# Optimization experiments

Measured on AMD Instinct MI355X. Metric: run time of the kernel, lower is better.

The kernel has to match this reference:

```python
import jax, jax.numpy as jnp
import numpy as np

D_MODEL = 768
D_INNER = 1536      # expand=2
D_STATE = 16
DT_RANK = 48        # ceil(768/16)
D_CONV = 4
DEPTH = 24
NUM_CLASSES = 527
GRID = (8, 64)      # (128/16, 1024/16)
SEQ = GRID[0] * GRID[1]
TOKPOS = SEQ // 2   # middle cls token position


def setup_inputs() -> dict:
    key = jax.random.key(0)
    ks = jax.random.split(key, 12)
    rn = lambda k, s, sc=0.02: jax.random.normal(k, s, jnp.float32) * sc
    A_init = jnp.log(jnp.arange(1, D_STATE + 1, dtype=jnp.float32))  # S4D-real init
    return {
        "x": jax.random.normal(ks[0], (1, 1, 128, 1024), jnp.float32),
        "patch_w": rn(ks[1], (D_MODEL, 1, 16, 16)),
        "patch_b": jnp.zeros((D_MODEL,), jnp.float32),
        "cls_token": rn(ks[2], (1, 1, D_MODEL)),
        "pos_embed": rn(ks[3], (1, SEQ + 1, D_MODEL)),
        "in_proj_w": rn(ks[4], (DEPTH, 2 * D_INNER, D_MODEL)),
        "conv_w": rn(ks[5], (DEPTH, 2, D_INNER, D_CONV), 0.1),
        "conv_b": jnp.zeros((DEPTH, 2, D_INNER), jnp.float32),
        "xproj_w": rn(ks[6], (DEPTH, 2, DT_RANK + 2 * D_STATE, D_INNER)),
        "dtproj_w": rn(ks[7], (DEPTH, 2, D_INNER, DT_RANK), 0.1),
        "dtproj_b": jnp.full((DEPTH, 2, D_INNER), float(np.log(np.expm1(0.01))), jnp.float32),
        "A_log": jnp.ones((DEPTH, 2, D_INNER, 1), jnp.float32) * A_init,
        "D_skip": jnp.ones((DEPTH, 2, D_INNER), jnp.float32),
        "out_proj_w": rn(ks[8], (DEPTH, D_MODEL, D_INNER)),
        "norm_w": jnp.ones((DEPTH, D_MODEL), jnp.float32),
        "norm_f_w": jnp.ones((D_MODEL,), jnp.float32),
        "head_w": rn(ks[9], (NUM_CLASSES, D_MODEL)),
        "head_b": jnp.zeros((NUM_CLASSES,), jnp.float32),
    }


def _rmsnorm(x, w, eps=1e-5):
    return x * jax.lax.rsqrt(jnp.mean(x * x, axis=-1, keepdims=True) + eps) * w


def _causal_conv_silu(x, w, b):
    # x [B,d,L], depthwise causal conv, kernel D_CONV, left-pad D_CONV-1
    L = x.shape[-1]
    xp = jnp.pad(x, ((0, 0), (0, 0), (D_CONV - 1, 0)))
    y = sum(w[:, k, None] * xp[:, :, k:k + L] for k in range(D_CONV)) + b[:, None]
    return jax.nn.silu(y)


def _selective_scan(dt, A, Bm, C, u):
    # dt,u: [B,d,L]; Bm,C: [B,N,L]; A: [d,N] (negative)
    def step(h, inp):
        dt_t, B_t, C_t, u_t = inp           # [B,d],[B,N],[B,N],[B,d]
        h = h * jnp.exp(dt_t[..., None] * A) + (dt_t * u_t)[..., None] * B_t[:, None, :]
        return h, jnp.einsum('bdn,bn->bd', h, C_t)
    h0 = jnp.zeros((dt.shape[0], A.shape[0], A.shape[1]), dt.dtype)
    mv = lambda a: jnp.moveaxis(a, -1, 0)
    _, ys = jax.lax.scan(step, h0, (mv(dt), mv(Bm), mv(C), mv(u)))
    return jnp.moveaxis(ys, 0, -1)          # [B,d,L]


def _mamba_dir(x, z, cw, cb, xw, dw, db, A_log, Dsk):
    xc = _causal_conv_silu(x, cw, cb)
    dbl = jnp.einsum('bdl,cd->bcl', xc, xw)                 # [B, R+2N, L]
    dt = jax.nn.softplus(jnp.einsum('brl,dr->bdl', dbl[:, :DT_RANK], dw) + db[:, None])
    Bm = dbl[:, DT_RANK:DT_RANK + D_STATE]
    C = dbl[:, DT_RANK + D_STATE:]
    y = _selective_scan(dt, -jnp.exp(A_log), Bm, C, xc) + Dsk[:, None] * xc
    return y * jax.nn.silu(z)


def _block(carry, p):
    hidden, residual = carry
    ipw, cw, cb, xw, dw, db, A_log, Dsk, opw, nw = p
    residual = residual + hidden                            # add -> norm -> mixer
    h = _rmsnorm(residual, nw)
    xz = jnp.einsum('bld,ed->ble', h, ipw)                  # [B,L,2*d_inner]
    x, z = jnp.split(jnp.moveaxis(xz, -1, 1), 2, axis=1)    # each [B,d_inner,L]
    yf = _mamba_dir(x, z, cw[0], cb[0], xw[0], dw[0], db[0], A_log[0], Dsk[0])
    yb = _mamba_dir(x[:, :, ::-1], z[:, :, ::-1], cw[1], cb[1], xw[1], dw[1],
                    db[1], A_log[1], Dsk[1])[:, :, ::-1]
    out = jnp.einsum('bdl,ed->ble', (yf + yb) * 0.5, opw)   # if_devide_out
    return (out, residual), None


def reference(x, patch_w, patch_b, cls_token, pos_embed, in_proj_w, conv_w, conv_b,
              xproj_w, dtproj_w, dtproj_b, A_log, D_skip, out_proj_w, norm_w,
              norm_f_w, head_w, head_b):
    h = jax.lax.conv_general_dilated(x, patch_w, (16, 16), 'VALID',
                                     dimension_numbers=('NCHW', 'OIHW', 'NCHW'))
    h = h + patch_b[None, :, None, None]
    B = h.shape[0]
    h = h.reshape(B, D_MODEL, SEQ).transpose(0, 2, 1)       # [B,512,768]
    cls = jnp.broadcast_to(cls_token, (B, 1, D_MODEL))
    h = jnp.concatenate([h[:, :TOKPOS], cls, h[:, TOKPOS:]], axis=1)  # [B,513,768]
    h = h + pos_embed
    carry = (h, jnp.zeros_like(h))
    (hidden, residual), _ = jax.lax.scan(
        _block, carry,
        (in_proj_w, conv_w, conv_b, xproj_w, dtproj_w, dtproj_b, A_log, D_skip,
         out_proj_w, norm_w))
    out = _rmsnorm(residual + hidden, norm_f_w)
    feat = out[:, TOKPOS]                                   # middle cls token
    return feat @ head_w.T + head_b
```

## Files before the change

kernel.cpp:

```cpp
#include <hip/hip_runtime.h>

#define L_SEQ 513
#define DM 768
#define DI 1536
#define DSTATE 16
#define DTRANK 48
#define NCLS 527
#define DEPTH 24
#define NC 32
#define CLEN 17
#define SKI 3
#define SKO 8

typedef unsigned short u16;
typedef __bf16 bf16x8 __attribute__((ext_vector_type(8)));
typedef float f32x4 __attribute__((ext_vector_type(4)));

#define MFMA_BF16(A, B, C) __builtin_amdgcn_mfma_f32_16x16x32_bf16(A, B, C, 0, 0, 0)

__device__ inline u16 f2bf(float x) {
  unsigned u = __float_as_uint(x);
  return (u16)((u + 0x7FFFu + ((u >> 16) & 1u)) >> 16);
}
__device__ inline float bf2f(u16 h) { return __uint_as_float((unsigned)h << 16); }
__device__ inline void split2(float v, u16& h, u16& l) {
  h = f2bf(v);
  l = f2bf(v - bf2f(h));
}
__device__ __forceinline__ int lofs(int row, int g) {
  int swz = (row & 3) ^ ((row >> 2) & 3);
  return row * 32 + ((g ^ swz) << 3);
}

__global__ void wconvert_kernel(const float* __restrict__ src,
                                u16* __restrict__ hi, u16* __restrict__ lo,
                                long n4) {
  long i = (long)blockIdx.x * 256 + threadIdx.x;
  long stride = (long)gridDim.x * 256;
  for (; i < n4; i += stride) {
    float4 v = ((const float4*)src)[i];
    ushort4 h, l;
    split2(v.x, h.x, l.x);
    split2(v.y, h.y, l.y);
    split2(v.z, h.z, l.z);
    split2(v.w, h.w, l.w);
    ((ushort4*)hi)[i] = h;
    ((ushort4*)lo)[i] = l;
  }
}

__global__ void patch_embed_kernel(const float* __restrict__ x,
                                   const float* __restrict__ pw,
                                   const float* __restrict__ pb,
                                   const float* __restrict__ cls,
                                   const float* __restrict__ pos,
                                   float* __restrict__ hidden,
                                   float* __restrict__ residual) {
  int c = blockIdx.x * 256 + threadIdx.x;
  int s = blockIdx.y;
  if (c >= DM) return;
  float val;
  if (s == 256) {
    val = cls[c];
  } else {
    int p = s - (s > 256 ? 1 : 0);
    int gy = p >> 6, gx = p & 63;
    const float* xp = x + gy * 16 * 1024 + gx * 16;
    const float* wp = pw + c * 256;
    float acc = pb[c];
#pragma unroll 4
    for (int ky = 0; ky < 16; ++ky)
#pragma unroll
      for (int kx = 0; kx < 16; ++kx)
        acc += xp[ky * 1024 + kx] * wp[ky * 16 + kx];
    val = acc;
  }
  long idx = (long)s * DM + c;
  hidden[idx] = val + pos[idx];
  residual[idx] = 0.f;
}

__global__ void rmsnorm_kernel(const float* __restrict__ hp, int nparts, long pstr,
                               float* __restrict__ residual,
                               u16* __restrict__ hnh, u16* __restrict__ hnl,
                               const float* __restrict__ w) {
  int t = blockIdx.x;
  float* rrow = residual + (long)t * DM;
  int tid = threadIdx.x;
  float vals[3];
  float ss = 0.f;
#pragma unroll
  for (int i = 0; i < 3; ++i) {
    int c = tid + i * 256;
    float v = rrow[c];
    for (int p = 0; p < nparts; ++p) v += hp[(long)p * pstr + (long)t * DM + c];
    vals[i] = v;
    rrow[c] = v;
    ss += v * v;
  }
#pragma unroll
  for (int o = 32; o; o >>= 1) ss += __shfl_down(ss, o, 64);
  __shared__ float sacc[4];
  if ((tid & 63) == 0) sacc[tid >> 6] = ss;
  __syncthreads();
  float tot = sacc[0] + sacc[1] + sacc[2] + sacc[3];
  float rs = rsqrtf(tot / (float)DM + 1e-5f);
#pragma unroll
  for (int i = 0; i < 3; ++i) {
    int c = tid + i * 256;
    float y = vals[i] * rs * w[c];
    u16 h, l;
    split2(y, h, l);
    hnh[(long)t * DM + c] = h;
    hnl[(long)t * DM + c] = l;
  }
}

template <int AMODE>
__global__ __launch_bounds__(256) void gemm128(
    const void* __restrict__ A0, const void* __restrict__ A1,
    const u16* __restrict__ Bh, const u16* __restrict__ Bl,
    float* __restrict__ C,
    int M, int N, int K, int lda, int ldb, int ldc,
    long sA, long sB, long sC, int NSK, int Kb, long sP) {
  int z = blockIdx.z;
  int batch = z / NSK, sk = z - batch * NSK;
  const u16* Ahb = nullptr;
  const u16* Alb = nullptr;
  const float* Af = nullptr;
  const float* Ag = nullptr;
  if (AMODE == 0) {
    Ahb = (const u16*)A0 + (long)batch * sA;
    Alb = (const u16*)A1 + (long)batch * sA;
  } else {
    Af = (const float*)A0 + (long)batch * sA;
    Ag = (const float*)A1 + (long)batch * sA;
  }
  const u16* Bhb = Bh + (long)batch * sB;
  const u16* Blb = Bl + (long)batch * sB;
  float* Cb = C + (long)batch * sC + (long)sk * sP;
  int ks0 = sk * Kb;
  int kend = min(ks0 + Kb, K);

  __shared__ u16 SA[2][2][128 * 32];
  __shared__ u16 SB[2][2][128 * 32];

  int tid = threadIdx.x;
  int m0 = blockIdx.y * 128, n0 = blockIdx.x * 128;

  int r0 = tid >> 2, g0 = tid & 3;
  int r1 = r0 + 64;
  int l0 = lofs(r0, g0), l1 = lofs(r1, g0);
  long aoff0 = (long)(m0 + r0) * lda, aoff1 = (long)(m0 + r1) * lda;
  long boff0 = (long)(n0 + r0) * ldb, boff1 = (long)(n0 + r1) * ldb;
  bool am0 = (m0 + r0) < M, am1 = (m0 + r1) < M;
  bool bm0 = (n0 + r0) < N, bm1 = (n0 + r1) < N;

  int lane = tid & 63, w = tid >> 6;
  int wr = w >> 1, wc = w & 1;
  int fr = lane & 15, kh = lane >> 4;
  int offA[4], offB[4];
#pragma unroll
  for (int i = 0; i < 4; ++i) {
    offA[i] = lofs(wr * 64 + i * 16 + fr, kh);
    offB[i] = lofs(wc * 64 + i * 16 + fr, kh);
  }

  uint4 a0h, a1h, a0l, a1l, b0h, b1h, b0l, b1l;
  auto loadA = [&](long rowoff, bool ok, int k_, uint4& hh, uint4& ll) {
    uint4 z4 = {0, 0, 0, 0};
    if (AMODE == 0) {
      hh = ok ? *(const uint4*)(Ahb + rowoff + k_) : z4;
      ll = ok ? *(const uint4*)(Alb + rowoff + k_) : z4;
    } else {
      if (!ok) { hh = z4; ll = z4; return; }
      float4 f0 = *(const float4*)(Af + rowoff + k_);
      float4 f1 = *(const float4*)(Af + rowoff + k_ + 4);
      float4 g0v = *(const float4*)(Ag + rowoff + k_);
      float4 g1v = *(const float4*)(Ag + rowoff + k_ + 4);
      u16 ha[8], la[8];
      split2(0.5f * (f0.x + g0v.x), ha[0], la[0]);
      split2(0.5f * (f0.y + g0v.y), ha[1], la[1]);
      split2(0.5f * (f0.z + g0v.z), ha[2], la[2]);
      split2(0.5f * (f0.w + g0v.w), ha[3], la[3]);
      split2(0.5f * (f1.x + g1v.x), ha[4], la[4]);
      split2(0.5f * (f1.y + g1v.y), ha[5], la[5]);
      split2(0.5f * (f1.z + g1v.z), ha[6], la[6]);
      split2(0.5f * (f1.w + g1v.w), ha[7], la[7]);
      hh = *(const uint4*)ha;
      ll = *(const uint4*)la;
    }
  };
  auto loadstep = [&](int kb) {
    int k_ = kb + g0 * 8;
    bool kk = (k_ + 8 <= kend);
    uint4 z4 = {0, 0, 0, 0};
    loadA(aoff0, kk && am0, k_, a0h, a0l);
    loadA(aoff1, kk && am1, k_, a1h, a1l);
    b0h = (kk && bm0) ? *(const uint4*)(Bhb + boff0 + k_) : z4;
    b1h = (kk && bm1) ? *(const uint4*)(Bhb + boff1 + k_) : z4;
    b0l = (kk && bm0) ? *(const uint4*)(Blb + boff0 + k_) : z4;
    b1l = (kk && bm1) ? *(const uint4*)(Blb + boff1 + k_) : z4;
  };
  auto writebuf = [&](int b) {
    *(uint4*)&SA[b][0][l0] = a0h;
    *(uint4*)&SA[b][0][l1] = a1h;
    *(uint4*)&SA[b][1][l0] = a0l;
    *(uint4*)&SA[b][1][l1] = a1l;
    *(uint4*)&SB[b][0][l0] = b0h;
    *(uint4*)&SB[b][0][l1] = b1h;
    *(uint4*)&SB[b][1][l0] = b0l;
    *(uint4*)&SB[b][1][l1] = b1l;
  };

  f32x4 acc[4][4] = {};
  int nst = (kend - ks0 + 31) >> 5;
  loadstep(ks0);
  writebuf(0);
  if (nst > 1) loadstep(ks0 + 32);
  __syncthreads();

  for (int s = 0; s < nst; ++s) {
    int b = s & 1;
    bf16x8 fah[4], fal[4], fbh[4], fbl[4];
#pragma unroll
    for (int i = 0; i < 4; ++i) {
      fah[i] = __builtin_bit_cast(bf16x8, *(const uint4*)&SA[b][0][offA[i]]);
      fal[i] = __builtin_bit_cast(bf16x8, *(const uint4*)&SA[b][1][offA[i]]);
      fbh[i] = __builtin_bit_cast(bf16x8, *(const uint4*)&SB[b][0][offB[i]]);
      fbl[i] = __builtin_bit_cast(bf16x8, *(const uint4*)&SB[b][1][offB[i]]);
    }
#pragma unroll
    for (int mi = 0; mi < 4; ++mi)
#pragma unroll
      for (int ni = 0; ni < 4; ++ni) {
        acc[mi][ni] = MFMA_BF16(fah[mi], fbh[ni], acc[mi][ni]);
        acc[mi][ni] = MFMA_BF16(fah[mi], fbl[ni], acc[mi][ni]);
        acc[mi][ni] = MFMA_BF16(fal[mi], fbh[ni], acc[mi][ni]);
      }
    if (s + 1 < nst) {
      writebuf(b ^ 1);
      if (s + 2 < nst) loadstep(ks0 + (s + 2) * 32);
    }
    __syncthreads();
  }

#pragma unroll
  for (int mi = 0; mi < 4; ++mi)
#pragma unroll
    for (int ni = 0; ni < 4; ++ni) {
      int n = n0 + wc * 64 + ni * 16 + fr;
      if (n >= N) continue;
#pragma unroll
      for (int r = 0; r < 4; ++r) {
        int m = m0 + wr * 64 + mi * 16 + kh * 4 + r;
        if (m >= M) continue;
        Cb[(long)m * ldc + n] = acc[mi][ni][r];
      }
    }
}

__global__ void conv_silu_kernel(const float* __restrict__ xz_p,
                                 const float* __restrict__ cw,
                                 const float* __restrict__ cb,
                                 float* __restrict__ xc,
                                 u16* __restrict__ xch, u16* __restrict__ xcl) {
  const long PZ = (long)L_SEQ * 2 * DI;
  int dir = blockIdx.y;
  int idx = blockIdx.x * 256 + threadIdx.x;
  if (idx >= L_SEQ * (DI / 4)) return;
  int d4 = idx % (DI / 4);
  int t = idx / (DI / 4);
  int d = d4 * 4;
  float wv[4][4];
#pragma unroll
  for (int j = 0; j < 4; ++j) {
    float4 wr = *(const float4*)(cw + ((long)dir * DI + d + j) * 4);
    wv[j][0] = wr.x; wv[j][1] = wr.y; wv[j][2] = wr.z; wv[j][3] = wr.w;
  }
  float4 bv = *(const float4*)(cb + (long)dir * DI + d);
  float a0 = bv.x, a1 = bv.y, a2 = bv.z, a3 = bv.w;
#pragma unroll
  for (int k = 0; k < 4; ++k) {
    int tau = t + k - 3;
    if (tau >= 0) {
      int tsrc = dir ? (L_SEQ - 1 - tau) : tau;
      long o = (long)tsrc * (2 * DI) + d;
      float4 x0 = *(const float4*)(xz_p + o);
      float4 x1 = *(const float4*)(xz_p + o + PZ);
      float4 x2 = *(const float4*)(xz_p + o + 2 * PZ);
      a0 += wv[0][k] * (x0.x + x1.x + x2.x);
      a1 += wv[1][k] * (x0.y + x1.y + x2.y);
      a2 += wv[2][k] * (x0.z + x1.z + x2.z);
      a3 += wv[3][k] * (x0.w + x1.w + x2.w);
    }
  }
  float4 sv;
  sv.x = a0 / (1.f + __expf(-a0));
  sv.y = a1 / (1.f + __expf(-a1));
  sv.z = a2 / (1.f + __expf(-a2));
  sv.w = a3 / (1.f + __expf(-a3));
  long o = ((long)dir * L_SEQ + t) * DI + d;
  *(float4*)(xc + o) = sv;
  ushort4 h, l;
  split2(sv.x, h.x, l.x);
  split2(sv.y, h.y, l.y);
  split2(sv.z, h.z, l.z);
  split2(sv.w, h.w, l.w);
  *(ushort4*)(xch + o) = h;
  *(ushort4*)(xcl + o) = l;
}

__global__ __launch_bounds__(256) void scan_all(
    const float* __restrict__ xc,
    const float* __restrict__ dbl,
    const float* __restrict__ xz_p,
    const float* __restrict__ dtw,
    const float* __restrict__ dtb,
    const float* __restrict__ A_log,
    const float* __restrict__ Dsk,
    float* __restrict__ y) {
  const long PZ = (long)L_SEQ * 2 * DI;
  int dir = blockIdx.y;
  int d0 = blockIdx.x * 8;
  int tid = threadIdx.x;
  __shared__ float Q[8][NC][DSTATE];
  __shared__ float Sv[8][NC];

  const float* xcp = xc + (long)dir * L_SEQ * DI;
  const float* dblp = dbl + (long)dir * L_SEQ * 80;

  int dl = tid & 7, c = tid >> 3;
  int d = d0 + dl;
  float negA[DSTATE];
#pragma unroll
  for (int n = 0; n < DSTATE; ++n)
    negA[n] = -__expf(A_log[((long)dir * DI + d) * DSTATE + n]);
  float4 dwr[12];
  {
    const float4* dwp = (const float4*)(dtw + ((long)dir * DI + d) * DTRANK);
#pragma unroll
    for (int q = 0; q < 12; ++q) dwr[q] = dwp[q];
  }
  float db_ = dtb[(long)dir * DI + d];

  int t0 = c * CLEN, t1 = min(t0 + CLEN, L_SEQ);

  {
    float h[DSTATE];
#pragma unroll
    for (int n = 0; n < DSTATE; ++n) h[n] = 0.f;
    float S = 0.f;
    for (int t = t0; t < t1; ++t) {
      const float4* R = (const float4*)(dblp + (long)t * 80);
      float dot = db_;
#pragma unroll
      for (int q = 0; q < 12; ++q) {
        float4 r4 = R[q];
        dot += r4.x * dwr[q].x + r4.y * dwr[q].y + r4.z * dwr[q].z + r4.w * dwr[q].w;
      }
      float dt = (dot > 20.f) ? dot : log1pf(__expf(dot));
      float u = xcp[(long)t * DI + d];
      float du = dt * u;
      S += dt;
      float4 b0 = R[12], b1 = R[13], b2 = R[14], b3 = R[15];
      float Bv[DSTATE] = {b0.x, b0.y, b0.z, b0.w, b1.x, b1.y, b1.z, b1.w,
                          b2.x, b2.y, b2.z, b2.w, b3.x, b3.y, b3.z, b3.w};
#pragma unroll
      for (int n = 0; n < DSTATE; ++n)
        h[n] = h[n] * __expf(dt * negA[n]) + du * Bv[n];
    }
    Sv[dl][c] = S;
#pragma unroll
    for (int n = 0; n < DSTATE; ++n) Q[dl][c][n] = h[n];
  }
  __syncthreads();
  if (tid < 128) {
    int fdl = tid >> 4, n = tid & 15;
    int fd = d0 + fdl;
    float nA = -__expf(A_log[((long)dir * DI + fd) * DSTATE + n]);
    float h = 0.f;
    for (int cc = 0; cc < NC; ++cc) {
      float S = Sv[fdl][cc];
      float q = Q[fdl][cc][n];
      Q[fdl][cc][n] = h;
      h = h * __expf(nA * S) + q;
    }
  }
  __syncthreads();
  {
    float h[DSTATE];
#pragma unroll
    for (int n = 0; n < DSTATE; ++n) h[n] = Q[dl][c][n];
    float dskip = Dsk[(long)dir * DI + d];
    for (int t = t0; t < t1; ++t) {
      const float4* R = (const float4*)(dblp + (long)t * 80);
      float dot = db_;
#pragma unroll
      for (int q = 0; q < 12; ++q) {
        float4 r4 = R[q];
        dot += r4.x * dwr[q].x + r4.y * dwr[q].y + r4.z * dwr[q].z + r4.w * dwr[q].w;
      }
      float dt = (dot > 20.f) ? dot : log1pf(__expf(dot));
      float u = xcp[(long)t * DI + d];
      float du = dt * u;
      float4 b0 = R[12], b1 = R[13], b2 = R[14], b3 = R[15];
      float4 c0 = R[16], c1 = R[17], c2 = R[18], c3 = R[19];
      float Bv[DSTATE] = {b0.x, b0.y, b0.z, b0.w, b1.x, b1.y, b1.z, b1.w,
                          b2.x, b2.y, b2.z, b2.w, b3.x, b3.y, b3.z, b3.w};
      float Cv[DSTATE] = {c0.x, c0.y, c0.z, c0.w, c1.x, c1.y, c1.z, c1.w,
                          c2.x, c2.y, c2.z, c2.w, c3.x, c3.y, c3.z, c3.w};
      float acc = 0.f;
#pragma unroll
      for (int n = 0; n < DSTATE; ++n) {
        h[n] = h[n] * __expf(dt * negA[n]) + du * Bv[n];
        acc += h[n] * Cv[n];
      }
      int tsrc = dir ? (L_SEQ - 1 - t) : t;
      long zo = (long)tsrc * (2 * DI) + DI + d;
      float zv = xz_p[zo] + xz_p[zo + PZ] + xz_p[zo + 2 * PZ];
      float sz = zv / (1.f + __expf(-zv));
      y[((long)dir * L_SEQ + tsrc) * DI + d] = (acc + dskip * u) * sz;
    }
  }
}

__global__ void head_kernel(const float* __restrict__ residual,
                            const float* __restrict__ hp, long pstr,
                            const float* __restrict__ nfw,
                            const float* __restrict__ hw,
                            const float* __restrict__ hb,
                            float* __restrict__ out) {
  int j = blockIdx.x;
  int tid = threadIdx.x;
  const float* r = residual + (long)256 * DM;
  float ss = 0.f, dp = 0.f;
#pragma unroll
  for (int i = 0; i < 3; ++i) {
    int c = tid + i * 256;
    float v = r[c];
    for (int p = 0; p < SKO; ++p) v += hp[(long)p * pstr + (long)256 * DM + c];
    ss += v * v;
    dp += v * nfw[c] * hw[(long)j * DM + c];
  }
#pragma unroll
  for (int o = 32; o; o >>= 1) {
    ss += __shfl_down(ss, o, 64);
    dp += __shfl_down(dp, o, 64);
  }
  __shared__ float s1[4], s2[4];
  if ((tid & 63) == 0) {
    s1[tid >> 6] = ss;
    s2[tid >> 6] = dp;
  }
  __syncthreads();
  if (tid == 0) {
    float tot = s1[0] + s1[1] + s1[2] + s1[3];
    float d = s2[0] + s2[1] + s2[2] + s2[3];
    out[j] = d * rsqrtf(tot / (float)DM + 1e-5f) + hb[j];
  }
}

extern "C" void kernel_launch(void* const* d_in, const int* in_sizes, int n_in,
                              void* d_out, int out_size, void* d_ws, size_t ws_size,
                              hipStream_t stream) {
  const float* x        = (const float*)d_in[0];
  const float* patch_w  = (const float*)d_in[1];
  const float* patch_b  = (const float*)d_in[2];
  const float* cls_tok  = (const float*)d_in[3];
  const float* pos_emb  = (const float*)d_in[4];
  const float* in_proj  = (const float*)d_in[5];
  const float* conv_w   = (const float*)d_in[6];
  const float* conv_b   = (const float*)d_in[7];
  const float* xproj_w  = (const float*)d_in[8];
  const float* dtproj_w = (const float*)d_in[9];
  const float* dtproj_b = (const float*)d_in[10];
  const float* A_log    = (const float*)d_in[11];
  const float* D_skip   = (const float*)d_in[12];
  const float* out_proj = (const float*)d_in[13];
  const float* norm_w   = (const float*)d_in[14];
  const float* norm_f_w = (const float*)d_in[15];
  const float* head_w   = (const float*)d_in[16];
  const float* head_b   = (const float*)d_in[17];
  float* out = (float*)d_out;

  const long PHN = (long)L_SEQ * DM;
  const long PZ  = (long)L_SEQ * 2 * DI;

  float* ws = (float*)d_ws;
  float* residual = ws; ws += PHN;
  float* xz_p     = ws; ws += SKI * PZ;
  float* xc       = ws; ws += (long)2 * L_SEQ * DI;
  float* dbl      = ws; ws += (long)2 * L_SEQ * 80;
  float* yb       = ws; ws += (long)2 * L_SEQ * DI;
  float* hid_p    = ws; ws += (long)SKO * PHN;

  u16* wsu = (u16*)ws;
  const long N_HN = PHN;
  const long N_XC = (long)2 * L_SEQ * DI;
  const long N_WI = (long)DEPTH * 2 * DI * DM;
  const long N_WX = (long)DEPTH * 2 * 80 * DI;
  const long N_WO = (long)DEPTH * DM * DI;
  u16* hn_h = wsu; wsu += N_HN;
  u16* hn_l = wsu; wsu += N_HN;
  u16* xc_h = wsu; wsu += N_XC;
  u16* xc_l = wsu; wsu += N_XC;
  u16* wi_h = wsu; wsu += N_WI;
  u16* wi_l = wsu; wsu += N_WI;
  u16* wx_h = wsu; wsu += N_WX;
  u16* wx_l = wsu; wsu += N_WX;
  u16* wo_h = wsu; wsu += N_WO;
  u16* wo_l = wsu; wsu += N_WO;

  wconvert_kernel<<<2048, 256, 0, stream>>>(in_proj,  wi_h, wi_l, N_WI / 4);
  wconvert_kernel<<<512,  256, 0, stream>>>(xproj_w,  wx_h, wx_l, N_WX / 4);
  wconvert_kernel<<<2048, 256, 0, stream>>>(out_proj, wo_h, wo_l, N_WO / 4);

  patch_embed_kernel<<<dim3(3, L_SEQ), 256, 0, stream>>>(
      x, patch_w, patch_b, cls_tok, pos_emb, hid_p, residual);

  for (int l = 0; l < DEPTH; ++l) {
    const u16* wih = wi_h + (long)l * 2 * DI * DM;
    const u16* wil = wi_l + (long)l * 2 * DI * DM;
    const u16* wxh = wx_h + (long)l * 2 * 80 * DI;
    const u16* wxl = wx_l + (long)l * 2 * 80 * DI;
    const u16* woh = wo_h + (long)l * DM * DI;
    const u16* wol = wo_l + (long)l * DM * DI;
    const float* cw  = conv_w   + (long)l * 2 * DI * 4;
    const float* cb  = conv_b   + (long)l * 2 * DI;
    const float* dw  = dtproj_w + (long)l * 2 * DI * DTRANK;
    const float* db  = dtproj_b + (long)l * 2 * DI;
    const float* Al  = A_log    + (long)l * 2 * DI * DSTATE;
    const float* Dk  = D_skip   + (long)l * 2 * DI;
    const float* nw  = norm_w   + (long)l * DM;

    rmsnorm_kernel<<<L_SEQ, 256, 0, stream>>>(
        hid_p, (l == 0) ? 1 : SKO, PHN, residual, hn_h, hn_l, nw);

    gemm128<0><<<dim3(24, 5, SKI), 256, 0, stream>>>(
        hn_h, hn_l, wih, wil, xz_p, L_SEQ, 2 * DI, DM, DM, DM, 2 * DI,
        0, 0, 0, SKI, DM / SKI, PZ);

    conv_silu_kernel<<<dim3(770, 2), 256, 0, stream>>>(xz_p, cw, cb, xc, xc_h, xc_l);

    gemm128<0><<<dim3(1, 5, 2), 256, 0, stream>>>(
        xc_h, xc_l, wxh, wxl, dbl, L_SEQ, 80, DI, DI, DI, 80,
        (long)L_SEQ * DI, (long)80 * DI, (long)L_SEQ * 80, 1, DI, 0);

    scan_all<<<dim3(DI / 8, 2), 256, 0, stream>>>(
        xc, dbl, xz_p, dw, db, Al, Dk, yb);

    gemm128<1><<<dim3(6, 5, SKO), 256, 0, stream>>>(
        yb, yb + (long)L_SEQ * DI, woh, wol, hid_p, L_SEQ, DM, DI, DI, DI, DM,
        0, 0, 0, SKO, DI / SKO, PHN);
  }

  head_kernel<<<NCLS, 256, 0, stream>>>(residual, hid_p, PHN,
                                        norm_f_w, head_w, head_b, out);
}
```

Baseline: 4.750 ms.

## Move dt projection to MFMA GEMM and precompute silu(z) before scan

The dt projection and softplus leave the scan kernel. They now run as a batched split-bf16 MFMA GEMM with a fused bias and softplus epilogue, fed by hi/lo copies that the x_proj GEMM epilogue emits. The conv kernel also computes silu(z) into a separate buffer, so the scan reads one value per step instead of summing split-K partials and applying silu. In-projection split-K drops from 3 to 2, which means fewer partial buffers to write and reduce but less parallelism. This adds an extra kernel launch and materializes a dt buffer of size 2×L×DI.

```diff
diff --git a/kernel.cpp b/kernel.cpp
--- a/kernel.cpp
+++ b/kernel.cpp
@@ -9,10 +9,11 @@
 #define DEPTH 24
 #define NC 32
 #define CLEN 17
-#define SKI 3
+#define SKI 2
 #define SKO 8
 
 typedef unsigned short u16;
+typedef unsigned int u32;
 typedef __bf16 bf16x8 __attribute__((ext_vector_type(8)));
 typedef float f32x4 __attribute__((ext_vector_type(4)));
 
@@ -31,119 +32,35 @@
   int swz = (row & 3) ^ ((row >> 2) & 3);
   return row * 32 + ((g ^ swz) << 3);
 }
-
-__global__ void wconvert_kernel(const float* __restrict__ src,
-                                u16* __restrict__ hi, u16* __restrict__ lo,
-                                long n4) {
-  long i = (long)blockIdx.x * 256 + threadIdx.x;
-  long stride = (long)gridDim.x * 256;
-  for (; i < n4; i += stride) {
-    float4 v = ((const float4*)src)[i];
-    ushort4 h, l;
-    split2(v.x, h.x, l.x);
-    split2(v.y, h.y, l.y);
-    split2(v.z, h.z, l.z);
-    split2(v.w, h.w, l.w);
-    ((ushort4*)hi)[i] = h;
-    ((ushort4*)lo)[i] = l;
-  }
-}
-
-__global__ void patch_embed_kernel(const float* __restrict__ x,
-                                   const float* __restrict__ pw,
-                                   const float* __restrict__ pb,
-                                   const float* __restrict__ cls,
-                                   const float* __restrict__ pos,
-                                   float* __restrict__ hidden,
-                                   float* __restrict__ residual) {
-  int c = blockIdx.x * 256 + threadIdx.x;
-  int s = blockIdx.y;
-  if (c >= DM) return;
-  float val;
-  if (s == 256) {
-    val = cls[c];
-  } else {
-    int p = s - (s > 256 ? 1 : 0);
-    int gy = p >> 6, gx = p & 63;
-    const float* xp = x + gy * 16 * 1024 + gx * 16;
-    const float* wp = pw + c * 256;
-    float acc = pb[c];
-#pragma unroll 4
-    for (int ky = 0; ky < 16; ++ky)
-#pragma unroll
-      for (int kx = 0; kx < 16; ++kx)
-        acc += xp[ky * 1024 + kx] * wp[ky * 16 + kx];
-    val = acc;
-  }
-  long idx = (long)s * DM + c;
-  hidden[idx] = val + pos[idx];
-  residual[idx] = 0.f;
-}
-
-__global__ void rmsnorm_kernel(const float* __restrict__ hp, int nparts, long pstr,
-                               float* __restrict__ residual,
-                               u16* __restrict__ hnh, u16* __restrict__ hnl,
-                               const float* __restrict__ w) {
-  int t = blockIdx.x;
-  float* rrow = residual + (long)t * DM;
-  int tid = threadIdx.x;
-  float vals[3];
-  float ss = 0.f;
-#pragma unroll
-  for (int i = 0; i < 3; ++i) {
-    int c = tid + i * 256;
-    float v = rrow[c];
-    for (int p = 0; p < nparts; ++p) v += hp[(long)p * pstr + (long)t * DM + c];
-    vals[i] = v;
-    rrow[c] = v;
-    ss += v * v;
-  }
-#pragma unroll
-  for (int o = 32; o; o >>= 1) ss += __shfl_down(ss, o, 64);
-  __shared__ float sacc[4];
-  if ((tid & 63) == 0) sacc[tid >> 6] = ss;
-  __syncthreads();
-  float tot = sacc[0] + sacc[1] + sacc[2] + sacc[3];
-  float rs = rsqrtf(tot / (float)DM + 1e-5f);
-#pragma unroll
-  for (int i = 0; i < 3; ++i) {
-    int c = tid + i * 256;
-    float y = vals[i] * rs * w[c];
-    u16 h, l;
-    split2(y, h, l);
-    hnh[(long)t * DM + c] = h;
-    hnl[(long)t * DM + c] = l;
-  }
-}
+__device__ inline float siluf(float v) { return v / (1.f + __expf(-v)); }
 
 template <int AMODE>
 __global__ __launch_bounds__(256) void gemm128(
-    const void* __restrict__ A0, const void* __restrict__ A1,
+    const void* A0, const void* A1,
     const u16* __restrict__ Bh, const u16* __restrict__ Bl,
     float* __restrict__ C,
     int M, int N, int K, int lda, int ldb, int ldc,
-    long sA, long sB, long sC, int NSK, int Kb, long sP) {
+    long sA, long sB, long sC, int NSK, int Kb, long sP,
+    const float* __restrict__ bias, long sBias, int act,
+    u16* __restrict__ Chi, u16* __restrict__ Clo, int ncap, int ldhl, long sChl) {
+  __shared__ __align__(16) u16 LDSU[32768];
+  u16* SA = LDSU;
+  u16* SB = LDSU + 16384;
+
   int z = blockIdx.z;
   int batch = z / NSK, sk = z - batch * NSK;
-  const u16* Ahb = nullptr;
-  const u16* Alb = nullptr;
-  const float* Af = nullptr;
-  const float* Ag = nullptr;
-  if (AMODE == 0) {
-    Ahb = (const u16*)A0 + (long)batch * sA;
-    Alb = (const u16*)A1 + (long)batch * sA;
-  } else {
-    Af = (const float*)A0 + (long)batch * sA;
-    Ag = (const float*)A1 + (long)batch * sA;
-  }
+  const u16* Ahb = (const u16*)A0 + (AMODE == 0 ? (long)batch * sA : 0);
+  const u16* Alb = (const u16*)A1 + (AMODE == 0 ? (long)batch * sA : 0);
+  const float* Af = (const float*)A0 + (AMODE == 1 ? (long)batch * sA : 0);
+  const float* Ag = (const float*)A1 + (AMODE == 1 ? (long)batch * sA : 0);
   const u16* Bhb = Bh + (long)batch * sB;
   const u16* Blb = Bl + (long)batch * sB;
   float* Cb = C + (long)batch * sC + (long)sk * sP;
+  const float* biasb = bias ? bias + (long)batch * sBias : nullptr;
+  u16* Chib = Chi ? Chi + (long)batch * sChl : nullptr;
+  u16* Clob = Clo ? Clo + (long)batch * sChl : nullptr;
   int ks0 = sk * Kb;
   int kend = min(ks0 + Kb, K);
-
-  __shared__ u16 SA[2][2][128 * 32];
-  __shared__ u16 SB[2][2][128 * 32];
 
   int tid = threadIdx.x;
   int m0 = blockIdx.y * 128, n0 = blockIdx.x * 128;
@@ -203,14 +120,14 @@
     b1l = (kk && bm1) ? *(const uint4*)(Blb + boff1 + k_) : z4;
   };
   auto writebuf = [&](int b) {
-    *(uint4*)&SA[b][0][l0] = a0h;
-    *(uint4*)&SA[b][0][l1] = a1h;
-    *(uint4*)&SA[b][1][l0] = a0l;
-    *(uint4*)&SA[b][1][l1] = a1l;
-    *(uint4*)&SB[b][0][l0] = b0h;
-    *(uint4*)&SB[b][0][l1] = b1h;
-    *(uint4*)&SB[b][1][l0] = b0l;
-    *(uint4*)&SB[b][1][l1] = b1l;
+    *(uint4*)&SA[((b << 1) | 0) * 4096 + l0] = a0h;
+    *(uint4*)&SA[((b << 1) | 0) * 4096 + l1] = a1h;
+    *(uint4*)&SA[((b << 1) | 1) * 4096 + l0] = a0l;
+    *(uint4*)&SA[((b << 1) | 1) * 4096 + l1] = a1l;
+    *(uint4*)&SB[((b << 1) | 0) * 4096 + l0] = b0h;
+    *(uint4*)&SB[((b << 1) | 0) * 4096 + l1] = b1h;
+    *(uint4*)&SB[((b << 1) | 1) * 4096 + l0] = b0l;
+    *(uint4*)&SB[((b << 1) | 1) * 4096 + l1] = b1l;
   };
 
   f32x4 acc[4][4] = {};
@@ -225,10 +142,10 @@
     bf16x8 fah[4], fal[4], fbh[4], fbl[4];
 #pragma unroll
     for (int i = 0; i < 4; ++i) {
-      fah[i] = __builtin_bit_cast(bf16x8, *(const uint4*)&SA[b][0][offA[i]]);
-      fal[i] = __builtin_bit_cast(bf16x8, *(const uint4*)&SA[b][1][offA[i]]);
-      fbh[i] = __builtin_bit_cast(bf16x8, *(const uint4*)&SB[b][0][offB[i]]);
-      fbl[i] = __builtin_bit_cast(bf16x8, *(const uint4*)&SB[b][1][offB[i]]);
+      fah[i] = __builtin_bit_cast(bf16x8, *(const uint4*)&SA[((b << 1) | 0) * 4096 + offA[i]]);
+      fal[i] = __builtin_bit_cast(bf16x8, *(const uint4*)&SA[((b << 1) | 1) * 4096 + offA[i]]);
+      fbh[i] = __builtin_bit_cast(bf16x8, *(const uint4*)&SB[((b << 1) | 0) * 4096 + offB[i]]);
+      fbl[i] = __builtin_bit_cast(bf16x8, *(const uint4*)&SB[((b << 1) | 1) * 4096 + offB[i]]);
     }
 #pragma unroll
     for (int mi = 0; mi < 4; ++mi)
@@ -251,128 +168,220 @@
     for (int ni = 0; ni < 4; ++ni) {
       int n = n0 + wc * 64 + ni * 16 + fr;
       if (n >= N) continue;
+      float bv = biasb ? biasb[n] : 0.f;
 #pragma unroll
       for (int r = 0; r < 4; ++r) {
         int m = m0 + wr * 64 + mi * 16 + kh * 4 + r;
         if (m >= M) continue;
-        Cb[(long)m * ldc + n] = acc[mi][ni][r];
+        float v = acc[mi][ni][r] + bv;
+        if (act == 1) v = (v > 20.f) ? v : log1pf(__expf(v));
+        Cb[(long)m * ldc + n] = v;
+        if (Chib && n < ncap) {
+          u16 hh, ll;
+          split2(v, hh, ll);
+          Chib[(long)m * ldhl + n] = hh;
+          Clob[(long)m * ldhl + n] = ll;
+        }
       }
     }
 }
 
-__global__ void conv_silu_kernel(const float* __restrict__ xz_p,
-                                 const float* __restrict__ cw,
-                                 const float* __restrict__ cb,
-                                 float* __restrict__ xc,
-                                 u16* __restrict__ xch, u16* __restrict__ xcl) {
+__global__ void wconvert_kernel(const float* __restrict__ src,
+                                u16* __restrict__ hi, u16* __restrict__ lo,
+                                long n4) {
+  long i = (long)blockIdx.x * 256 + threadIdx.x;
+  long stride = (long)gridDim.x * 256;
+  for (; i < n4; i += stride) {
+    float4 v = ((const float4*)src)[i];
+    ushort4 h, l;
+    split2(v.x, h.x, l.x);
+    split2(v.y, h.y, l.y);
+    split2(v.z, h.z, l.z);
+    split2(v.w, h.w, l.w);
+    ((ushort4*)hi)[i] = h;
+    ((ushort4*)lo)[i] = l;
+  }
+}
+
+__global__ void patch_embed_kernel(const float* __restrict__ x,
+                                   const float* __restrict__ pw,
+                                   const float* __restrict__ pb,
+                                   const float* __restrict__ cls,
+                                   const float* __restrict__ pos,
+                                   float* __restrict__ hidden,
+                                   float* __restrict__ residual) {
+  int c = blockIdx.x * 256 + threadIdx.x;
+  int s = blockIdx.y;
+  if (c >= DM) return;
+  float val;
+  if (s == 256) {
+    val = cls[c];
+  } else {
+    int p = s - (s > 256 ? 1 : 0);
+    int gy = p >> 6, gx = p & 63;
+    const float* xp = x + gy * 16 * 1024 + gx * 16;
+    const float* wp = pw + c * 256;
+    float acc = pb[c];
+#pragma unroll 4
+    for (int ky = 0; ky < 16; ++ky)
+#pragma unroll
+      for (int kx = 0; kx < 16; ++kx)
+        acc += xp[ky * 1024 + kx] * wp[ky * 16 + kx];
+    val = acc;
+  }
+  long idx = (long)s * DM + c;
+  hidden[idx] = val + pos[idx];
+  residual[idx] = 0.f;
+}
+
+__global__ void rmsnorm_kernel(const float* __restrict__ hp, int nparts, long pstr,
+                               float* __restrict__ residual,
+                               u16* __restrict__ hnh, u16* __restrict__ hnl,
+                               const float* __restrict__ w) {
+  int t = blockIdx.x;
+  float* rrow = residual + (long)t * DM;
+  int tid = threadIdx.x;
+  float vals[3];
+  float ss = 0.f;
+#pragma unroll
+  for (int i = 0; i < 3; ++i) {
+    int c = tid + i * 256;
+    float v = rrow[c];
+    for (int p = 0; p < nparts; ++p) v += hp[(long)p * pstr + (long)t * DM + c];
+    vals[i] = v;
+    rrow[c] = v;
+    ss += v * v;
+  }
+#pragma unroll
+  for (int o = 32; o; o >>= 1) ss += __shfl_down(ss, o, 64);
+  __shared__ float sacc[4];
+  if ((tid & 63) == 0) sacc[tid >> 6] = ss;
+  __syncthreads();
+  float tot = sacc[0] + sacc[1] + sacc[2] + sacc[3];
+  float rs = rsqrtf(tot / (float)DM + 1e-5f);
+#pragma unroll
+  for (int i = 0; i < 3; ++i) {
+    int c = tid + i * 256;
+    float y = vals[i] * rs * w[c];
+    u16 h, l;
+    split2(y, h, l);
+    hnh[(long)t * DM + c] = h;
+    hnl[(long)t * DM + c] = l;
+  }
+}
+
+__global__ void conv_zs_kernel(const float* __restrict__ xz_p,
+                               const float* __restrict__ cw,
+                               const float* __restrict__ cb,
+                               float* __restrict__ xc,
+                               u16* __restrict__ xch, u16* __restrict__ xcl,
+                               float* __restrict__ zs) {
   const long PZ = (long)L_SEQ * 2 * DI;
-  int dir = blockIdx.y;
-  int idx = blockIdx.x * 256 + threadIdx.x;
-  if (idx >= L_SEQ * (DI / 4)) return;
-  int d4 = idx % (DI / 4);
-  int t = idx / (DI / 4);
-  int d = d4 * 4;
-  float wv[4][4];
-#pragma unroll
-  for (int j = 0; j < 4; ++j) {
-    float4 wr = *(const float4*)(cw + ((long)dir * DI + d + j) * 4);
-    wv[j][0] = wr.x; wv[j][1] = wr.y; wv[j][2] = wr.z; wv[j][3] = wr.w;
-  }
-  float4 bv = *(const float4*)(cb + (long)dir * DI + d);
-  float a0 = bv.x, a1 = bv.y, a2 = bv.z, a3 = bv.w;
-#pragma unroll
-  for (int k = 0; k < 4; ++k) {
-    int tau = t + k - 3;
-    if (tau >= 0) {
-      int tsrc = dir ? (L_SEQ - 1 - tau) : tau;
-      long o = (long)tsrc * (2 * DI) + d;
-      float4 x0 = *(const float4*)(xz_p + o);
-      float4 x1 = *(const float4*)(xz_p + o + PZ);
-      float4 x2 = *(const float4*)(xz_p + o + 2 * PZ);
-      a0 += wv[0][k] * (x0.x + x1.x + x2.x);
-      a1 += wv[1][k] * (x0.y + x1.y + x2.y);
-      a2 += wv[2][k] * (x0.z + x1.z + x2.z);
-      a3 += wv[3][k] * (x0.w + x1.w + x2.w);
-    }
-  }
-  float4 sv;
-  sv.x = a0 / (1.f + __expf(-a0));
-  sv.y = a1 / (1.f + __expf(-a1));
-  sv.z = a2 / (1.f + __expf(-a2));
-  sv.w = a3 / (1.f + __expf(-a3));
-  long o = ((long)dir * L_SEQ + t) * DI + d;
-  *(float4*)(xc + o) = sv;
-  ushort4 h, l;
-  split2(sv.x, h.x, l.x);
-  split2(sv.y, h.y, l.y);
-  split2(sv.z, h.z, l.z);
-  split2(sv.w, h.w, l.w);
-  *(ushort4*)(xch + o) = h;
-  *(ushort4*)(xcl + o) = l;
+  int v = blockIdx.x;
+  int tid = threadIdx.x;
+  if (v < 1540) {
+    int dir = v / 770, vv = v - dir * 770;
+    int idx = vv * 256 + tid;
+    if (idx >= L_SEQ * (DI / 4)) return;
+    int d4 = idx % (DI / 4);
+    int t = idx / (DI / 4);
+    int d = d4 * 4;
+    float wv[4][4];
+#pragma unroll
+    for (int j = 0; j < 4; ++j) {
+      float4 wr4 = *(const float4*)(cw + ((long)dir * DI + d + j) * 4);
+      wv[j][0] = wr4.x; wv[j][1] = wr4.y; wv[j][2] = wr4.z; wv[j][3] = wr4.w;
+    }
+    float4 bv = *(const float4*)(cb + (long)dir * DI + d);
+    float a0 = bv.x, a1 = bv.y, a2 = bv.z, a3 = bv.w;
+#pragma unroll
+    for (int k = 0; k < 4; ++k) {
+      int tau = t + k - 3;
+      if (tau >= 0) {
+        int tsrc = dir ? (L_SEQ - 1 - tau) : tau;
+        long o = (long)tsrc * (2 * DI) + d;
+        float4 x0 = *(const float4*)(xz_p + o);
+        float4 x1 = *(const float4*)(xz_p + o + PZ);
+        a0 += wv[0][k] * (x0.x + x1.x);
+        a1 += wv[1][k] * (x0.y + x1.y);
+        a2 += wv[2][k] * (x0.z + x1.z);
+        a3 += wv[3][k] * (x0.w + x1.w);
+      }
+    }
+    float4 sv;
+    sv.x = siluf(a0); sv.y = siluf(a1); sv.z = siluf(a2); sv.w = siluf(a3);
+    long o = ((long)dir * L_SEQ + t) * DI + d;
+    *(float4*)(xc + o) = sv;
+    ushort4 h, lo;
+    split2(sv.x, h.x, lo.x);
+    split2(sv.y, h.y, lo.y);
+    split2(sv.z, h.z, lo.z);
+    split2(sv.w, h.w, lo.w);
+    *(ushort4*)(xch + o) = h;
+    *(ushort4*)(xcl + o) = lo;
+  } else {
+    int vv = v - 1540;
+    int idx = vv * 256 + tid;
+    if (idx >= L_SEQ * (DI / 4)) return;
+    int d4 = idx % (DI / 4);
+    int t = idx / (DI / 4);
+    long zo = (long)t * (2 * DI) + DI + d4 * 4;
+    float4 z0 = *(const float4*)(xz_p + zo);
+    float4 z1 = *(const float4*)(xz_p + zo + PZ);
+    float4 sv;
+    sv.x = siluf(z0.x + z1.x);
+    sv.y = siluf(z0.y + z1.y);
+    sv.z = siluf(z0.z + z1.z);
+    sv.w = siluf(z0.w + z1.w);
+    *(float4*)(zs + (long)t * DI + d4 * 4) = sv;
+  }
 }
 
 __global__ __launch_bounds__(256) void scan_all(
+    const float* __restrict__ dtb,
     const float* __restrict__ xc,
     const float* __restrict__ dbl,
-    const float* __restrict__ xz_p,
-    const float* __restrict__ dtw,
-    const float* __restrict__ dtb,
+    const float* __restrict__ zs,
     const float* __restrict__ A_log,
     const float* __restrict__ Dsk,
     float* __restrict__ y) {
-  const long PZ = (long)L_SEQ * 2 * DI;
+  __shared__ float Q[8 * NC * DSTATE];
+  __shared__ float Sv[8 * NC];
+  const long LDIlen = (long)L_SEQ * DI;
   int dir = blockIdx.y;
   int d0 = blockIdx.x * 8;
   int tid = threadIdx.x;
-  __shared__ float Q[8][NC][DSTATE];
-  __shared__ float Sv[8][NC];
-
-  const float* xcp = xc + (long)dir * L_SEQ * DI;
+  const float* dtp = dtb + dir * LDIlen;
+  const float* xcp = xc + dir * LDIlen;
   const float* dblp = dbl + (long)dir * L_SEQ * 80;
-
   int dl = tid & 7, c = tid >> 3;
   int d = d0 + dl;
   float negA[DSTATE];
 #pragma unroll
   for (int n = 0; n < DSTATE; ++n)
     negA[n] = -__expf(A_log[((long)dir * DI + d) * DSTATE + n]);
-  float4 dwr[12];
-  {
-    const float4* dwp = (const float4*)(dtw + ((long)dir * DI + d) * DTRANK);
-#pragma unroll
-    for (int q = 0; q < 12; ++q) dwr[q] = dwp[q];
-  }
-  float db_ = dtb[(long)dir * DI + d];
-
   int t0 = c * CLEN, t1 = min(t0 + CLEN, L_SEQ);
-
   {
     float h[DSTATE];
 #pragma unroll
     for (int n = 0; n < DSTATE; ++n) h[n] = 0.f;
     float S = 0.f;
     for (int t = t0; t < t1; ++t) {
-      const float4* R = (const float4*)(dblp + (long)t * 80);
-      float dot = db_;
-#pragma unroll
-      for (int q = 0; q < 12; ++q) {
-        float4 r4 = R[q];
-        dot += r4.x * dwr[q].x + r4.y * dwr[q].y + r4.z * dwr[q].z + r4.w * dwr[q].w;
-      }
-      float dt = (dot > 20.f) ? dot : log1pf(__expf(dot));
+      float dt = dtp[(long)t * DI + d];
       float u = xcp[(long)t * DI + d];
       float du = dt * u;
       S += dt;
-      float4 b0 = R[12], b1 = R[13], b2 = R[14], b3 = R[15];
+      const float4* B4 = (const float4*)(dblp + (long)t * 80 + DTRANK);
+      float4 b0 = B4[0], b1 = B4[1], b2 = B4[2], b3 = B4[3];
       float Bv[DSTATE] = {b0.x, b0.y, b0.z, b0.w, b1.x, b1.y, b1.z, b1.w,
                           b2.x, b2.y, b2.z, b2.w, b3.x, b3.y, b3.z, b3.w};
 #pragma unroll
       for (int n = 0; n < DSTATE; ++n)
         h[n] = h[n] * __expf(dt * negA[n]) + du * Bv[n];
     }
-    Sv[dl][c] = S;
-#pragma unroll
-    for (int n = 0; n < DSTATE; ++n) Q[dl][c][n] = h[n];
+    Sv[dl * NC + c] = S;
+#pragma unroll
+    for (int n = 0; n < DSTATE; ++n) Q[(dl * NC + c) * DSTATE + n] = h[n];
   }
   __syncthreads();
   if (tid < 128) {
@@ -381,9 +390,9 @@
     float nA = -__expf(A_log[((long)dir * DI + fd) * DSTATE + n]);
     float h = 0.f;
     for (int cc = 0; cc < NC; ++cc) {
-      float S = Sv[fdl][cc];
-      float q = Q[fdl][cc][n];
-      Q[fdl][cc][n] = h;
+      float S = Sv[fdl * NC + cc];
+      float q = Q[(fdl * NC + cc) * DSTATE + n];
+      Q[(fdl * NC + cc) * DSTATE + n] = h;
       h = h * __expf(nA * S) + q;
     }
   }
@@ -391,21 +400,15 @@
   {
     float h[DSTATE];
 #pragma unroll
-    for (int n = 0; n < DSTATE; ++n) h[n] = Q[dl][c][n];
+    for (int n = 0; n < DSTATE; ++n) h[n] = Q[(dl * NC + c) * DSTATE + n];
     float dskip = Dsk[(long)dir * DI + d];
     for (int t = t0; t < t1; ++t) {
-      const float4* R = (const float4*)(dblp + (long)t * 80);
-      float dot = db_;
-#pragma unroll
-      for (int q = 0; q < 12; ++q) {
-        float4 r4 = R[q];
-        dot += r4.x * dwr[q].x + r4.y * dwr[q].y + r4.z * dwr[q].z + r4.w * dwr[q].w;
-      }
-      float dt = (dot > 20.f) ? dot : log1pf(__expf(dot));
+      float dt = dtp[(long)t * DI + d];
       float u = xcp[(long)t * DI + d];
       float du = dt * u;
-      float4 b0 = R[12], b1 = R[13], b2 = R[14], b3 = R[15];
-      float4 c0 = R[16], c1 = R[17], c2 = R[18], c3 = R[19];
+      const float4* B4 = (const float4*)(dblp + (long)t * 80 + DTRANK);
+      float4 b0 = B4[0], b1 = B4[1], b2 = B4[2], b3 = B4[3];
+      float4 c0 = B4[4], c1 = B4[5], c2 = B4[6], c3 = B4[7];
       float Bv[DSTATE] = {b0.x, b0.y, b0.z, b0.w, b1.x, b1.y, b1.z, b1.w,
                           b2.x, b2.y, b2.z, b2.w, b3.x, b3.y, b3.z, b3.w};
       float Cv[DSTATE] = {c0.x, c0.y, c0.z, c0.w, c1.x, c1.y, c1.z, c1.w,
@@ -417,9 +420,7 @@
         acc += h[n] * Cv[n];
       }
       int tsrc = dir ? (L_SEQ - 1 - t) : t;
-      long zo = (long)tsrc * (2 * DI) + DI + d;
-      float zv = xz_p[zo] + xz_p[zo + PZ] + xz_p[zo + 2 * PZ];
-      float sz = zv / (1.f + __expf(-zv));
+      float sz = zs[(long)tsrc * DI + d];
       y[((long)dir * L_SEQ + tsrc) * DI + d] = (acc + dskip * u) * sz;
     }
   }
@@ -486,34 +487,44 @@
 
   const long PHN = (long)L_SEQ * DM;
   const long PZ  = (long)L_SEQ * 2 * DI;
-
-  float* ws = (float*)d_ws;
-  float* residual = ws; ws += PHN;
-  float* xz_p     = ws; ws += SKI * PZ;
-  float* xc       = ws; ws += (long)2 * L_SEQ * DI;
-  float* dbl      = ws; ws += (long)2 * L_SEQ * 80;
-  float* yb       = ws; ws += (long)2 * L_SEQ * DI;
-  float* hid_p    = ws; ws += (long)SKO * PHN;
-
-  u16* wsu = (u16*)ws;
+  const long LDIlen = (long)L_SEQ * DI;
+
+  float* fb = (float*)d_ws;
+  float* residual = fb; fb += PHN;
+  float* xz_p     = fb; fb += SKI * PZ;
+  float* xc       = fb; fb += (long)2 * LDIlen;
+  float* zs       = fb; fb += LDIlen;
+  float* dbl      = fb; fb += (long)2 * L_SEQ * 80;
+  float* dtb      = fb; fb += (long)2 * LDIlen;
+  float* yb       = fb; fb += (long)2 * LDIlen;
+  float* hid_p    = fb; fb += (long)SKO * PHN;
+
+  u16* wsu = (u16*)fb;
   const long N_HN = PHN;
-  const long N_XC = (long)2 * L_SEQ * DI;
+  const long N_XC = (long)2 * LDIlen;
+  const long N_D48 = (long)2 * L_SEQ * DTRANK;
   const long N_WI = (long)DEPTH * 2 * DI * DM;
   const long N_WX = (long)DEPTH * 2 * 80 * DI;
+  const long N_WD = (long)DEPTH * 2 * DI * DTRANK;
   const long N_WO = (long)DEPTH * DM * DI;
   u16* hn_h = wsu; wsu += N_HN;
   u16* hn_l = wsu; wsu += N_HN;
   u16* xc_h = wsu; wsu += N_XC;
   u16* xc_l = wsu; wsu += N_XC;
+  u16* d48_h = wsu; wsu += N_D48;
+  u16* d48_l = wsu; wsu += N_D48;
   u16* wi_h = wsu; wsu += N_WI;
   u16* wi_l = wsu; wsu += N_WI;
   u16* wx_h = wsu; wsu += N_WX;
   u16* wx_l = wsu; wsu += N_WX;
+  u16* wd_h = wsu; wsu += N_WD;
+  u16* wd_l = wsu; wsu += N_WD;
   u16* wo_h = wsu; wsu += N_WO;
   u16* wo_l = wsu; wsu += N_WO;
 
   wconvert_kernel<<<2048, 256, 0, stream>>>(in_proj,  wi_h, wi_l, N_WI / 4);
   wconvert_kernel<<<512,  256, 0, stream>>>(xproj_w,  wx_h, wx_l, N_WX / 4);
+  wconvert_kernel<<<512,  256, 0, stream>>>(dtproj_w, wd_h, wd_l, N_WD / 4);
   wconvert_kernel<<<2048, 256, 0, stream>>>(out_proj, wo_h, wo_l, N_WO / 4);
 
   patch_embed_kernel<<<dim3(3, L_SEQ), 256, 0, stream>>>(
@@ -524,35 +535,43 @@
     const u16* wil = wi_l + (long)l * 2 * DI * DM;
     const u16* wxh = wx_h + (long)l * 2 * 80 * DI;
     const u16* wxl = wx_l + (long)l * 2 * 80 * DI;
+    const u16* wdh = wd_h + (long)l * 2 * DI * DTRANK;
+    const u16* wdl = wd_l + (long)l * 2 * DI * DTRANK;
     const u16* woh = wo_h + (long)l * DM * DI;
     const u16* wol = wo_l + (long)l * DM * DI;
-    const float* cw  = conv_w   + (long)l * 2 * DI * 4;
-    const float* cb  = conv_b   + (long)l * 2 * DI;
-    const float* dw  = dtproj_w + (long)l * 2 * DI * DTRANK;
-    const float* db  = dtproj_b + (long)l * 2 * DI;
-    const float* Al  = A_log    + (long)l * 2 * DI * DSTATE;
-    const float* Dk  = D_skip   + (long)l * 2 * DI;
-    const float* nw  = norm_w   + (long)l * DM;
+    const float* cw = conv_w + (long)l * 2 * DI * 4;
+    const float* cb = conv_b + (long)l * 2 * DI;
+    const float* db = dtproj_b + (long)l * 2 * DI;
+    const float* Al = A_log + (long)l * 2 * DI * DSTATE;
+    const float* Dk = D_skip + (long)l * 2 * DI;
+    const float* nw = norm_w + (long)l * DM;
 
     rmsnorm_kernel<<<L_SEQ, 256, 0, stream>>>(
         hid_p, (l == 0) ? 1 : SKO, PHN, residual, hn_h, hn_l, nw);
 
     gemm128<0><<<dim3(24, 5, SKI), 256, 0, stream>>>(
         hn_h, hn_l, wih, wil, xz_p, L_SEQ, 2 * DI, DM, DM, DM, 2 * DI,
-        0, 0, 0, SKI, DM / SKI, PZ);
-
-    conv_silu_kernel<<<dim3(770, 2), 256, 0, stream>>>(xz_p, cw, cb, xc, xc_h, xc_l);
+        0, 0, 0, SKI, DM / SKI, PZ,
+        nullptr, 0, 0, nullptr, nullptr, 0, 0, 0);
+
+    conv_zs_kernel<<<2310, 256, 0, stream>>>(xz_p, cw, cb, xc, xc_h, xc_l, zs);
 
     gemm128<0><<<dim3(1, 5, 2), 256, 0, stream>>>(
         xc_h, xc_l, wxh, wxl, dbl, L_SEQ, 80, DI, DI, DI, 80,
-        (long)L_SEQ * DI, (long)80 * DI, (long)L_SEQ * 80, 1, DI, 0);
-
-    scan_all<<<dim3(DI / 8, 2), 256, 0, stream>>>(
-        xc, dbl, xz_p, dw, db, Al, Dk, yb);
+        LDIlen, (long)80 * DI, (long)L_SEQ * 80, 1, DI, 0,
+        nullptr, 0, 0, d48_h, d48_l, DTRANK, DTRANK, (long)L_SEQ * DTRANK);
+
+    gemm128<0><<<dim3(12, 5, 2), 256, 0, stream>>>(
+        d48_h, d48_l, wdh, wdl, dtb, L_SEQ, DI, DTRANK, DTRANK, DTRANK, DI,
+        (long)L_SEQ * DTRANK, (long)DI * DTRANK, LDIlen, 1, DTRANK, 0,
+        db, DI, 1, nullptr, nullptr, 0, 0, 0);
+
+    scan_all<<<dim3(192, 2), 256, 0, stream>>>(dtb, xc, dbl, zs, Al, Dk, yb);
 
     gemm128<1><<<dim3(6, 5, SKO), 256, 0, stream>>>(
-        yb, yb + (long)L_SEQ * DI, woh, wol, hid_p, L_SEQ, DM, DI, DI, DI, DM,
-        0, 0, 0, SKO, DI / SKO, PHN);
+        yb, yb + LDIlen, woh, wol, hid_p, L_SEQ, DM, DI, DI, DI, DM,
+        0, 0, 0, SKO, DI / SKO, PHN,
+        nullptr, 0, 0, nullptr, nullptr, 0, 0, 0);
   }
 
   head_kernel<<<NCLS, 256, 0, stream>>>(residual, hid_p, PHN,
```

Measured after the change: 5.207 ms. 1.1x slower.
